# Kernel optimization log

Hardware: AMD Instinct MI355X
Metric: run time of the kernel (lower is better)

Reference implementation:

```python
import jax, jax.numpy as jnp
import numpy as np


def setup_inputs() -> dict:
    key = jax.random.key(0)
    images = jax.random.uniform(key, (64, 384, 384, 3), dtype=jnp.float32)
    return {"images": images, "k": 5}


def reference(images, k):
    # cv2.dilate with a k x k kernel of ones == per-channel max filter with SAME padding.
    # Applied over the whole batch in one fused reduce_window (window only over H, W).
    out = jax.lax.reduce_window(
        images,
        -jnp.inf,
        jax.lax.max,
        window_dimensions=(1, k, k, 1),
        window_strides=(1, 1, 1, 1),
        padding="SAME",
    )
    # cv_to_tf appends a trailing singleton dim before tf.stack -> (B, H, W, C, 1)
    return out[..., None]
```

## Files before the change

kernel.cpp:

```cpp
#include <hip/hip_runtime.h>


#define Bn 64
#define H 384
#define ROWBYTES 4608
#define WF4 288
#define RB 12
#define NLOAD (RB + 4)
#define GROUPS 8
#define STRIPS 5
#define SOUT 60
#define NBLK (Bn * GROUPS * STRIPS)
#define NEGINF (-3.402823466e+38f)

typedef float f32x4 __attribute__((ext_vector_type(4)));

template <int I> struct Ic { static constexpr int v = I; };
template <int I, int N, class F>
__device__ __forceinline__ void static_for(F f) {
  if constexpr (I < N) {
    f(Ic<I>{});
    static_for<I + 1, N>(f);
  }
}

__device__ __forceinline__ f32x4 gload4_async(const char* p) {
  f32x4 r;
  asm volatile("global_load_dwordx4 %0, %1, off" : "=&v"(r) : "v"(p));
  return r;
}

template <int N>
__device__ __forceinline__ void vm_wait() {
  __builtin_amdgcn_sched_barrier(0);
  asm volatile("s_waitcnt vmcnt(%0)" ::"n"(N) : "memory");
  __builtin_amdgcn_sched_barrier(0);
}

__device__ __forceinline__ f32x4 max4(f32x4 a, f32x4 b) {
  f32x4 r;
  r.x = fmaxf(a.x, b.x); r.y = fmaxf(a.y, b.y);
  r.z = fmaxf(a.z, b.z); r.w = fmaxf(a.w, b.w);
  return r;
}

__global__ __launch_bounds__(256, 4) void dilate5_kernel(
    const float* __restrict__ in, float* __restrict__ out) {
  const int wv = threadIdx.x >> 6;
  const int lane = threadIdx.x & 63;

  const int orig = blockIdx.x;
  int t = (orig & 7) * (NBLK / 8) + (orig >> 3);
  const int strip = t % STRIPS; t /= STRIPS;
  const int grp = t % GROUPS;   t /= GROUPS;
  const int b = t;

  const int row0 = (grp * 4 + wv) * RB;
  const int col = strip * SOUT - 2 + lane;
  const bool cvalid = (col >= 0) && (col < WF4);
  const int ccl = col < 0 ? 0 : (col > WF4 - 1 ? WF4 - 1 : col);
  const size_t coff = (size_t)ccl * 16;
  const bool willstore = (lane >= 2) && (lane < 62) && (col < WF4);

  const char* __restrict__ imgb = (const char*)in + (size_t)b * H * ROWBYTES;
  char* __restrict__ outb = (char*)out + (size_t)b * H * ROWBYTES;

  f32x4 raw[NLOAD];
#pragma unroll
  for (int j = 0; j < NLOAD; ++j) {
    int gh = row0 - 2 + j;
    int ghc = gh < 0 ? 0 : (gh > H - 1 ? H - 1 : gh);
    raw[j] = gload4_async(imgb + (size_t)ghc * ROWBYTES + coff);
  }

  static_for<0, RB>([&](auto ic) {
    constexpr int i = decltype(ic)::v;
    vm_wait<(NLOAD - 1) - (i + 4)>();

    f32x4 v = max4(max4(max4(raw[i], raw[i + 1]), max4(raw[i + 2], raw[i + 3])),
                   raw[i + 4]);
    if (!cvalid) { v.x = NEGINF; v.y = NEGINF; v.z = NEGINF; v.w = NEGINF; }

    float Bx = __shfl_up(v.x, 1), By = __shfl_up(v.y, 1);
    float Bz = __shfl_up(v.z, 1), Bw = __shfl_up(v.w, 1);
    float Dx = __shfl_down(v.x, 1), Dy = __shfl_down(v.y, 1);
    float Dz = __shfl_down(v.z, 1), Dw = __shfl_down(v.w, 1);
    float Az = __shfl_up(v.z, 2), Aw = __shfl_up(v.w, 2);
    float Ex = __shfl_down(v.x, 2), Ey = __shfl_down(v.y, 2);
    f32x4 h;
    h.x = fmaxf(fmaxf(fmaxf(Az, By), fmaxf(v.x, v.w)), Dz);
    h.y = fmaxf(fmaxf(fmaxf(Aw, Bz), fmaxf(v.y, Dx)), Dw);
    h.z = fmaxf(fmaxf(fmaxf(Bx, Bw), fmaxf(v.z, Dy)), Ex);
    h.w = fmaxf(fmaxf(fmaxf(By, v.x), fmaxf(v.w, Dz)), Ey);

    if (willstore)
      __builtin_nontemporal_store(
          h, reinterpret_cast<f32x4*>(outb + (size_t)(row0 + i) * ROWBYTES + coff));
  });
}

extern "C" void kernel_launch(void* const* d_in, const int* in_sizes, int n_in,
                              void* d_out, int out_size, void* d_ws, size_t ws_size,
                              hipStream_t stream) {
  const float* images = (const float*)d_in[0];
  float* out = (float*)d_out;
  dilate5_kernel<<<NBLK, 256, 0, stream>>>(images, out);
}
```

Baseline: 203.2 us.

## Stage input rows through an LDS ring buffer via async global-to-LDS loads

Each block now covers a full-width band of 24 rows and streams input rows into an 8-slot LDS ring using global_load_lds, prefetching 7 rows ahead. Five waves then read the vertical 5-row window from LDS. This removes the redundant per-wave halo row loads and the register-held window. In exchange it adds two block barriers per row and drops the nontemporal stores, and the hand-tuned vmcnt wait schedule is fragile.

```diff
diff --git a/kernel.cpp b/kernel.cpp
--- a/kernel.cpp
+++ b/kernel.cpp
@@ -3,14 +3,13 @@
 
 #define Bn 64
 #define H 384
-#define ROWBYTES 4608
+#define ROWB 4608
 #define WF4 288
-#define RB 12
-#define NLOAD (RB + 4)
-#define GROUPS 8
-#define STRIPS 5
-#define SOUT 60
-#define NBLK (Bn * GROUPS * STRIPS)
+#define RB 24
+#define NIN (RB + 4)
+#define BANDS (H / RB)
+#define NBLK (Bn * BANDS)
+#define NTHR 320
 #define NEGINF (-3.402823466e+38f)
 
 typedef float f32x4 __attribute__((ext_vector_type(4)));
@@ -24,17 +23,16 @@
   }
 }
 
-__device__ __forceinline__ f32x4 gload4_async(const char* p) {
-  f32x4 r;
-  asm volatile("global_load_dwordx4 %0, %1, off" : "=&v"(r) : "v"(p));
-  return r;
-}
-
 template <int N>
 __device__ __forceinline__ void vm_wait() {
   __builtin_amdgcn_sched_barrier(0);
   asm volatile("s_waitcnt vmcnt(%0)" ::"n"(N) : "memory");
   __builtin_amdgcn_sched_barrier(0);
+}
+
+__host__ __device__ constexpr int NW(int k) {
+  return k == 0 ? 3 : k == 1 ? 4 : k == 2 ? 5 : k <= 20 ? 6
+       : k == 21 ? 5 : k == 22 ? 4 : 3;
 }
 
 __device__ __forceinline__ f32x4 max4(f32x4 a, f32x4 b) {
@@ -44,41 +42,55 @@
   return r;
 }
 
-__global__ __launch_bounds__(256, 4) void dilate5_kernel(
+__global__ __launch_bounds__(NTHR, 5) void dilate5_kernel(
     const float* __restrict__ in, float* __restrict__ out) {
-  const int wv = threadIdx.x >> 6;
-  const int lane = threadIdx.x & 63;
+  __shared__ f32x4 ring[8][WF4];
+
+  const int t = threadIdx.x;
+  const int wv = t >> 6;
+  const int lane = t & 63;
 
   const int orig = blockIdx.x;
-  int t = (orig & 7) * (NBLK / 8) + (orig >> 3);
-  const int strip = t % STRIPS; t /= STRIPS;
-  const int grp = t % GROUPS;   t /= GROUPS;
-  const int b = t;
+  const int q = (orig & 7) * (NBLK / 8) + (orig >> 3);
+  const int band = q % BANDS;
+  const int b = q / BANDS;
+  const int r0 = band * RB;
 
-  const int row0 = (grp * 4 + wv) * RB;
-  const int col = strip * SOUT - 2 + lane;
+  const char* __restrict__ imgb = (const char*)in + (size_t)b * H * ROWB;
+  char* __restrict__ outb = (char*)out + (size_t)b * H * ROWB;
+
+  const int soff = wv * 1024 + lane * 16;
+  const bool sact = soff < ROWB;
+  char* lds0 = (char*)&ring[0][0];
+
+  auto stage = [&](int j) {
+    int gh = r0 - 2 + j;
+    gh = gh < 0 ? 0 : (gh > H - 1 ? H - 1 : gh);
+    const char* src = imgb + (size_t)gh * ROWB + soff;
+    char* dst = lds0 + (size_t)(j & 7) * ROWB + soff;
+    if (sact)
+      __builtin_amdgcn_global_load_lds(
+          (const __attribute__((address_space(1))) void*)src,
+          (__attribute__((address_space(3))) void*)dst, 16, 0, 0);
+  };
+
+  const int col = wv * 60 - 2 + lane;
   const bool cvalid = (col >= 0) && (col < WF4);
   const int ccl = col < 0 ? 0 : (col > WF4 - 1 ? WF4 - 1 : col);
-  const size_t coff = (size_t)ccl * 16;
   const bool willstore = (lane >= 2) && (lane < 62) && (col < WF4);
 
-  const char* __restrict__ imgb = (const char*)in + (size_t)b * H * ROWBYTES;
-  char* __restrict__ outb = (char*)out + (size_t)b * H * ROWBYTES;
-
-  f32x4 raw[NLOAD];
 #pragma unroll
-  for (int j = 0; j < NLOAD; ++j) {
-    int gh = row0 - 2 + j;
-    int ghc = gh < 0 ? 0 : (gh > H - 1 ? H - 1 : gh);
-    raw[j] = gload4_async(imgb + (size_t)ghc * ROWBYTES + coff);
-  }
+  for (int j = 0; j < 7; ++j) stage(j);
 
   static_for<0, RB>([&](auto ic) {
-    constexpr int i = decltype(ic)::v;
-    vm_wait<(NLOAD - 1) - (i + 4)>();
+    constexpr int k = decltype(ic)::v;
+    if constexpr (k <= 20) stage(k + 7);
+    vm_wait<NW(k)>();
+    __builtin_amdgcn_s_barrier();
 
-    f32x4 v = max4(max4(max4(raw[i], raw[i + 1]), max4(raw[i + 2], raw[i + 3])),
-                   raw[i + 4]);
+    f32x4 v = max4(max4(max4(ring[(k + 0) & 7][ccl], ring[(k + 1) & 7][ccl]),
+                        max4(ring[(k + 2) & 7][ccl], ring[(k + 3) & 7][ccl])),
+                   ring[(k + 4) & 7][ccl]);
     if (!cvalid) { v.x = NEGINF; v.y = NEGINF; v.z = NEGINF; v.w = NEGINF; }
 
     float Bx = __shfl_up(v.x, 1), By = __shfl_up(v.y, 1);
@@ -94,8 +106,10 @@
     h.w = fmaxf(fmaxf(fmaxf(By, v.x), fmaxf(v.w, Dz)), Ey);
 
     if (willstore)
-      __builtin_nontemporal_store(
-          h, reinterpret_cast<f32x4*>(outb + (size_t)(row0 + i) * ROWBYTES + coff));
+      *reinterpret_cast<f32x4*>(outb + (size_t)(r0 + k) * ROWB +
+                                (size_t)col * 16) = h;
+
+    __builtin_amdgcn_s_barrier();
   });
 }
 
@@ -104,5 +118,5 @@
                               hipStream_t stream) {
   const float* images = (const float*)d_in[0];
   float* out = (float*)d_out;
-  dilate5_kernel<<<NBLK, 256, 0, stream>>>(images, out);
+  dilate5_kernel<<<NBLK, NTHR, 0, stream>>>(images, out);
 }
```

Result: no change. 206.4 us (+1.6%).

## Replace row-strip register reuse with per-row tasks loading five rows each

Applied to the files above, without the earlier changes.

Each wave now processes 15 independent (row, segment) tasks. Every task loads its own five vertical neighbor rows. The old scheme loaded 16 rows once per wave and reused them across 12 output rows with hand-scheduled asm loads and waitcnts. Occupancy goes up (launch bounds 8, fewer registers) and the explicit async pipelining is dropped, at the cost of about 5x redundant global loads that the caches must absorb.

```diff
diff --git a/kernel.cpp b/kernel.cpp
--- a/kernel.cpp
+++ b/kernel.cpp
@@ -3,39 +3,15 @@
 
 #define Bn 64
 #define H 384
-#define ROWBYTES 4608
+#define ROWB 4608
 #define WF4 288
-#define RB 12
-#define NLOAD (RB + 4)
-#define GROUPS 8
-#define STRIPS 5
-#define SOUT 60
-#define NBLK (Bn * GROUPS * STRIPS)
+#define SEGS 5
+#define TPW 15
+#define NTHR 256
+#define NBLK 2048
 #define NEGINF (-3.402823466e+38f)
 
 typedef float f32x4 __attribute__((ext_vector_type(4)));
-
-template <int I> struct Ic { static constexpr int v = I; };
-template <int I, int N, class F>
-__device__ __forceinline__ void static_for(F f) {
-  if constexpr (I < N) {
-    f(Ic<I>{});
-    static_for<I + 1, N>(f);
-  }
-}
-
-__device__ __forceinline__ f32x4 gload4_async(const char* p) {
-  f32x4 r;
-  asm volatile("global_load_dwordx4 %0, %1, off" : "=&v"(r) : "v"(p));
-  return r;
-}
-
-template <int N>
-__device__ __forceinline__ void vm_wait() {
-  __builtin_amdgcn_sched_barrier(0);
-  asm volatile("s_waitcnt vmcnt(%0)" ::"n"(N) : "memory");
-  __builtin_amdgcn_sched_barrier(0);
-}
 
 __device__ __forceinline__ f32x4 max4(f32x4 a, f32x4 b) {
   f32x4 r;
@@ -44,41 +20,43 @@
   return r;
 }
 
-__global__ __launch_bounds__(256, 4) void dilate5_kernel(
+__global__ __launch_bounds__(NTHR, 8) void dilate5_kernel(
     const float* __restrict__ in, float* __restrict__ out) {
   const int wv = threadIdx.x >> 6;
   const int lane = threadIdx.x & 63;
 
   const int orig = blockIdx.x;
-  int t = (orig & 7) * (NBLK / 8) + (orig >> 3);
-  const int strip = t % STRIPS; t /= STRIPS;
-  const int grp = t % GROUPS;   t /= GROUPS;
-  const int b = t;
+  const int bid = (orig & 7) * (NBLK / 8) + (orig >> 3);
 
-  const int row0 = (grp * 4 + wv) * RB;
-  const int col = strip * SOUT - 2 + lane;
-  const bool cvalid = (col >= 0) && (col < WF4);
-  const int ccl = col < 0 ? 0 : (col > WF4 - 1 ? WF4 - 1 : col);
-  const size_t coff = (size_t)ccl * 16;
-  const bool willstore = (lane >= 2) && (lane < 62) && (col < WF4);
+  const int tau0 = (bid * 4 + wv) * TPW;
 
-  const char* __restrict__ imgb = (const char*)in + (size_t)b * H * ROWBYTES;
-  char* __restrict__ outb = (char*)out + (size_t)b * H * ROWBYTES;
+#pragma unroll
+  for (int t = 0; t < TPW; ++t) {
+    const int tau = tau0 + t;
+    const int seg = tau % SEGS;
+    const int rr = tau / SEGS;
+    const int row = rr % H;
+    const int b = rr / H;
 
-  f32x4 raw[NLOAD];
-#pragma unroll
-  for (int j = 0; j < NLOAD; ++j) {
-    int gh = row0 - 2 + j;
-    int ghc = gh < 0 ? 0 : (gh > H - 1 ? H - 1 : gh);
-    raw[j] = gload4_async(imgb + (size_t)ghc * ROWBYTES + coff);
-  }
+    const int col = seg * 60 - 2 + lane;
+    const bool cvalid = (col >= 0) && (col < WF4);
+    const int ccl = col < 0 ? 0 : (col > WF4 - 1 ? WF4 - 1 : col);
+    const bool willstore = (lane >= 2) && (lane < 62) && (col < WF4);
 
-  static_for<0, RB>([&](auto ic) {
-    constexpr int i = decltype(ic)::v;
-    vm_wait<(NLOAD - 1) - (i + 4)>();
+    const char* __restrict__ imgb = (const char*)in + (size_t)b * H * ROWB;
+    const size_t coff = (size_t)ccl * 16;
 
-    f32x4 v = max4(max4(max4(raw[i], raw[i + 1]), max4(raw[i + 2], raw[i + 3])),
-                   raw[i + 4]);
+    int r0 = row - 2; r0 = r0 < 0 ? 0 : r0;
+    int r1 = row - 1; r1 = r1 < 0 ? 0 : r1;
+    int r3 = row + 1; r3 = r3 > H - 1 ? H - 1 : r3;
+    int r4 = row + 2; r4 = r4 > H - 1 ? H - 1 : r4;
+    f32x4 w0 = *reinterpret_cast<const f32x4*>(imgb + (size_t)r0 * ROWB + coff);
+    f32x4 w1 = *reinterpret_cast<const f32x4*>(imgb + (size_t)r1 * ROWB + coff);
+    f32x4 w2 = *reinterpret_cast<const f32x4*>(imgb + (size_t)row * ROWB + coff);
+    f32x4 w3 = *reinterpret_cast<const f32x4*>(imgb + (size_t)r3 * ROWB + coff);
+    f32x4 w4 = *reinterpret_cast<const f32x4*>(imgb + (size_t)r4 * ROWB + coff);
+
+    f32x4 v = max4(max4(max4(w0, w1), max4(w2, w3)), w4);
     if (!cvalid) { v.x = NEGINF; v.y = NEGINF; v.z = NEGINF; v.w = NEGINF; }
 
     float Bx = __shfl_up(v.x, 1), By = __shfl_up(v.y, 1);
@@ -95,8 +73,9 @@
 
     if (willstore)
       __builtin_nontemporal_store(
-          h, reinterpret_cast<f32x4*>(outb + (size_t)(row0 + i) * ROWBYTES + coff));
-  });
+          h, reinterpret_cast<f32x4*>((char*)out + (size_t)b * H * ROWB +
+                                      (size_t)row * ROWB + (size_t)col * 16));
+  }
 }
 
 extern "C" void kernel_launch(void* const* d_in, const int* in_sizes, int n_in,
@@ -104,5 +83,5 @@
                               hipStream_t stream) {
   const float* images = (const float*)d_in[0];
   float* out = (float*)d_out;
-  dilate5_kernel<<<NBLK, 256, 0, stream>>>(images, out);
+  dilate5_kernel<<<NBLK, NTHR, 0, stream>>>(images, out);
 }
```

Result: slower. 225.0 us (+10.7%).
